# Kernel optimization log

Hardware: AMD Instinct MI355X
Metric: run time of the kernel (lower is better)

Reference implementation:

```python
import jax, jax.numpy as jnp
import numpy as np

B, L, H, NL, O = 16, 96, 256, 2, 32  # batch, window len, hidden, layers, horizon


def setup_inputs() -> dict:
    key = jax.random.key(0)
    ks = jax.random.split(key, 12)
    s = 1.0 / np.sqrt(H)  # torch LSTM/Linear init scale
    u = lambda k, shp: jax.random.uniform(k, shp, jnp.float32, -s, s)
    return dict(
        x_enc=jax.random.normal(ks[0], (B, L, 1), jnp.float32),
        x_mark_enc=jnp.zeros((1,), jnp.float32),
        x_dec=jnp.zeros((1,), jnp.float32),
        x_mark_dec=jnp.zeros((1,), jnp.float32),
        Wih0=u(ks[1], (4 * H, 1)), Whh0=u(ks[2], (4 * H, H)),
        bih0=u(ks[3], (4 * H,)), bhh0=u(ks[4], (4 * H,)),
        Wih1=u(ks[5], (4 * H, H)), Whh1=u(ks[6], (4 * H, H)),
        bih1=u(ks[7], (4 * H,)), bhh1=u(ks[8], (4 * H,)),
        fc_w=u(ks[9], (1, H)), fc_b=u(ks[10], (1,)),
    )


def _lstm(x, h, c, params):
    """Multi-layer LSTM over x [B,T,in]; h,c: [NL,B,H]. Returns final (h,c).
    Only the final hidden state is needed (out[:, -1] == h[-1])."""
    def cell(carry, x_t):
        h, c = carry
        inp = x_t
        hs, cs = [], []
        for l, (Wih, Whh, bih, bhh) in enumerate(params):
            gates = inp @ Wih.T + h[l] @ Whh.T + bih + bhh  # [B,4H], torch gate order i,f,g,o
            i, f, g, o = jnp.split(gates, 4, axis=-1)
            cn = jax.nn.sigmoid(f) * c[l] + jax.nn.sigmoid(i) * jnp.tanh(g)
            hn = jax.nn.sigmoid(o) * jnp.tanh(cn)
            hs.append(hn); cs.append(cn)
            inp = hn
        return (jnp.stack(hs), jnp.stack(cs)), None
    (h, c), _ = jax.lax.scan(jax.checkpoint(cell), (h, c), jnp.swapaxes(x, 0, 1))
    return h, c


def reference(x_enc, x_mark_enc, x_dec, x_mark_dec,
              Wih0, Whh0, bih0, bhh0, Wih1, Whh1, bih1, bhh1, fc_w, fc_b):
    params = ((Wih0, Whh0, bih0, bhh0), (Wih1, Whh1, bih1, bhh1))
    b, l = x_enc.shape[0], x_enc.shape[1]
    h0 = jnp.zeros((NL, b, H), x_enc.dtype)
    # warm-up pass over the full encoder window (output discarded, state kept)
    h, c = _lstm(x_enc, h0, h0, params)

    def step(carry, _):
        h, c, win = carry
        h, c = _lstm(win, h, c, params)          # re-run LSTM over full rolling window
        pred = h[-1] @ fc_w.T + fc_b              # [B,1]
        win = jnp.concatenate([win[:, 1:], pred[:, None, :]], axis=1)
        return (h, c, win), pred

    _, preds = jax.lax.scan(step, (h, c, x_enc), None, length=O)  # [O,B,1]
    out = jnp.zeros((b, l, 1), x_enc.dtype).at[:, :O, :].set(jnp.swapaxes(preds, 0, 1))
    return out
```

## Files before the change

kernel.cpp:

```cpp
#include <hip/hip_runtime.h>


#define NWG 96
#define LASTP 3169

__device__ __forceinline__ float sigm(float x) { return 1.0f / (1.0f + expf(-x)); }

__global__ void init_kernel(float* __restrict__ out, float* __restrict__ ws) {
  int i = blockIdx.x * blockDim.x + threadIdx.x;
  if (i < 16 * 96) out[i] = 0.0f;
  for (int j = i; j < 17056; j += gridDim.x * blockDim.x) ws[j] = 0.0f;
}

__global__ __launch_bounds__(256, 1) void lstm_coop(
    const float* __restrict__ x_enc,
    const float* __restrict__ Wih0, const float* __restrict__ Whh0,
    const float* __restrict__ bih0, const float* __restrict__ bhh0,
    const float* __restrict__ Wih1, const float* __restrict__ Whh1,
    const float* __restrict__ bih1, const float* __restrict__ bhh1,
    const float* __restrict__ fc_w, const float* __restrict__ fc_b,
    float* __restrict__ out, float* __restrict__ ws) {
  const int w = blockIdx.x;
  const int tid = threadIdx.x;
  const int wave = tid >> 6, lane = tid & 63;
  const int b = lane & 15, q = lane >> 4;

  float* h0buf = ws;
  float* h1buf = ws + 8192;
  float* predbuf = ws + 16384;
  unsigned* bar = (unsigned*)(ws + 17024);

  __shared__ float wlds[32 * 272];

  const bool isL0 = (w < 32);
  const int u = w - 32;

  if (isL0) {
    for (int i = 0; i < 32; ++i) {
      int r_w = i & 7, wv = i >> 3;
      int col = w * 8 + wv * 2 + (r_w >> 2), gate = r_w & 3;
      wlds[i * 272 + (tid >> 6) * 68 + (tid & 63)] = Whh0[(gate * 256 + col) * 256 + tid];
    }
  } else {
    for (int i = 0; i < 32; ++i) {
      int r_w = i & 7, wv = i >> 3;
      int col = u * 4 + wv, gate = r_w & 3;
      const float* Wsrc = (r_w >> 2) ? Whh1 : Wih1;
      wlds[i * 272 + (tid >> 6) * 68 + (tid & 63)] = Wsrc[(gate * 256 + col) * 256 + tid];
    }
  }

  float biasv[8], xw[8];
  if (isL0) {
#pragma unroll
    for (int r = 0; r < 8; ++r) {
      int col = w * 8 + wave * 2 + (r >> 2), gate = r & 3;
      int grow = gate * 256 + col;
      biasv[r] = bih0[grow] + bhh0[grow];
      xw[r] = Wih0[grow];
    }
  } else {
#pragma unroll
    for (int g = 0; g < 4; ++g) {
      int col = u * 4 + wave;
      int grow = g * 256 + col;
      biasv[g] = bih1[grow] + bhh1[grow];
      xw[g] = 0.0f;
    }
#pragma unroll
    for (int g = 4; g < 8; ++g) { biasv[g] = 0.0f; xw[g] = 0.0f; }
  }
  __syncthreads();

  double c0a = 0.0, c0b = 0.0, c1 = 0.0;
  const int colBaseL0 = w * 8 + wave * 2;
  const int colL1 = u * 4 + wave;

  for (int p = 0; p <= LASTP; ++p) {
    if (isL0) {
      if (p <= 3167) {
        const float* hsrc = h0buf + ((p + 1) & 1) * 4096 + b * 256 + q * 64;
        float h[64];
#pragma unroll
        for (int jj = 0; jj < 16; ++jj) {
          float4 v = *(const float4*)(hsrc + jj * 4);
          h[jj * 4 + 0] = v.x; h[jj * 4 + 1] = v.y; h[jj * 4 + 2] = v.z; h[jj * 4 + 3] = v.w;
        }
        float acc[8];
#pragma unroll
        for (int r = 0; r < 8; ++r) acc[r] = 0.0f;
#pragma unroll
        for (int r = 0; r < 8; ++r) {
          int base = (wave * 8 + r) * 272 + q * 68;
#pragma unroll
          for (int jj = 0; jj < 16; ++jj) {
            float4 wv = *(const float4*)&wlds[base + jj * 4];
            acc[r] += wv.x * h[jj * 4] + wv.y * h[jj * 4 + 1] + wv.z * h[jj * 4 + 2] + wv.w * h[jj * 4 + 3];
          }
        }
#pragma unroll
        for (int r = 0; r < 8; ++r) {
          acc[r] += __shfl_xor(acc[r], 16);
          acc[r] += __shfl_xor(acc[r], 32);
        }
        if (q == 0) {
          float xv;
          {
            int s = p;
            if (s < 96) {
              xv = x_enc[b * 96 + s];
            } else {
              int sk = s - 96;
              int k = sk / 96;
              int t = sk - k * 96;
              xv = (t < 96 - k) ? x_enc[b * 96 + k + t] : predbuf[(t - 96 + k) * 16 + b];
            }
          }
          float hv0, hv1;
          {
            float gi = acc[0] + xv * xw[0] + biasv[0];
            float gf = acc[1] + xv * xw[1] + biasv[1];
            float gg = acc[2] + xv * xw[2] + biasv[2];
            float go = acc[3] + xv * xw[3] + biasv[3];
            double cn = (double)sigm(gf) * c0a + (double)(sigm(gi) * tanhf(gg));
            hv0 = sigm(go) * tanhf((float)cn);
            c0a = cn;
          }
          {
            float gi = acc[4] + xv * xw[4] + biasv[4];
            float gf = acc[5] + xv * xw[5] + biasv[5];
            float gg = acc[6] + xv * xw[6] + biasv[6];
            float go = acc[7] + xv * xw[7] + biasv[7];
            double cn = (double)sigm(gf) * c0b + (double)(sigm(gi) * tanhf(gg));
            hv1 = sigm(go) * tanhf((float)cn);
            c0b = cn;
          }
          *(float2*)(h0buf + (p & 1) * 4096 + b * 256 + colBaseL0) = make_float2(hv0, hv1);
        }
      }
      if (w == 0 && wave == 0 && p >= 193 && ((p - 193) % 96) == 0) {
        int jp = (p - 193) / 96;
        if (jp < 32) {
          const float* hsrc = h1buf + 4096 + b * 256 + q * 64;
          const float* fw = fc_w + q * 64;
          float acc = 0.0f;
#pragma unroll
          for (int jj = 0; jj < 16; ++jj) {
            float4 hv = *(const float4*)(hsrc + jj * 4);
            float4 wv = *(const float4*)(fw + jj * 4);
            acc += hv.x * wv.x + hv.y * wv.y + hv.z * wv.z + hv.w * wv.w;
          }
          acc += __shfl_xor(acc, 16);
          acc += __shfl_xor(acc, 32);
          if (q == 0) {
            float pv = acc + fc_b[0];
            predbuf[jp * 16 + b] = pv;
            out[b * 96 + jp] = pv;
          }
        }
      }
    } else {
      if (p >= 1 && p <= 3168) {
        const float* h0src = h0buf + ((p + 1) & 1) * 4096 + b * 256 + q * 64;
        const float* h1src = h1buf + (p & 1) * 4096 + b * 256 + q * 64;
        float ha[64], hb[64];
#pragma unroll
        for (int jj = 0; jj < 16; ++jj) {
          float4 v = *(const float4*)(h0src + jj * 4);
          ha[jj * 4 + 0] = v.x; ha[jj * 4 + 1] = v.y; ha[jj * 4 + 2] = v.z; ha[jj * 4 + 3] = v.w;
        }
#pragma unroll
        for (int jj = 0; jj < 16; ++jj) {
          float4 v = *(const float4*)(h1src + jj * 4);
          hb[jj * 4 + 0] = v.x; hb[jj * 4 + 1] = v.y; hb[jj * 4 + 2] = v.z; hb[jj * 4 + 3] = v.w;
        }
        float acc[8];
#pragma unroll
        for (int r = 0; r < 8; ++r) acc[r] = 0.0f;
#pragma unroll
        for (int r = 0; r < 4; ++r) {
          int base = (wave * 8 + r) * 272 + q * 68;
#pragma unroll
          for (int jj = 0; jj < 16; ++jj) {
            float4 wv = *(const float4*)&wlds[base + jj * 4];
            acc[r] += wv.x * ha[jj * 4] + wv.y * ha[jj * 4 + 1] + wv.z * ha[jj * 4 + 2] + wv.w * ha[jj * 4 + 3];
          }
        }
#pragma unroll
        for (int r = 4; r < 8; ++r) {
          int base = (wave * 8 + r) * 272 + q * 68;
#pragma unroll
          for (int jj = 0; jj < 16; ++jj) {
            float4 wv = *(const float4*)&wlds[base + jj * 4];
            acc[r] += wv.x * hb[jj * 4] + wv.y * hb[jj * 4 + 1] + wv.z * hb[jj * 4 + 2] + wv.w * hb[jj * 4 + 3];
          }
        }
#pragma unroll
        for (int r = 0; r < 8; ++r) {
          acc[r] += __shfl_xor(acc[r], 16);
          acc[r] += __shfl_xor(acc[r], 32);
        }
        if (q == 0) {
          float gi = acc[0] + acc[4] + biasv[0];
          float gf = acc[1] + acc[5] + biasv[1];
          float gg = acc[2] + acc[6] + biasv[2];
          float go = acc[3] + acc[7] + biasv[3];
          double cn = (double)sigm(gf) * c1 + (double)(sigm(gi) * tanhf(gg));
          float hn = sigm(go) * tanhf((float)cn);
          c1 = cn;
          h1buf[((p + 1) & 1) * 4096 + b * 256 + colL1] = hn;
        }
      }
    }

    __syncthreads();
    if (tid == 0) {
      unsigned arrived = __hip_atomic_fetch_add(&bar[0], 1u, __ATOMIC_ACQ_REL, __HIP_MEMORY_SCOPE_AGENT);
      if (arrived == NWG - 1) {
        __hip_atomic_store(&bar[0], 0u, __ATOMIC_RELAXED, __HIP_MEMORY_SCOPE_AGENT);
        __hip_atomic_store(&bar[1], (unsigned)(p + 1), __ATOMIC_RELEASE, __HIP_MEMORY_SCOPE_AGENT);
      } else {
        while (__hip_atomic_load(&bar[1], __ATOMIC_RELAXED, __HIP_MEMORY_SCOPE_AGENT) < (unsigned)(p + 1)) {}
        __threadfence();
      }
    }
    __syncthreads();
  }
}

extern "C" void kernel_launch(void* const* d_in, const int* in_sizes, int n_in,
                              void* d_out, int out_size, void* d_ws, size_t ws_size,
                              hipStream_t stream) {
  const float* x_enc = (const float*)d_in[0];
  const float* Wih0 = (const float*)d_in[4];
  const float* Whh0 = (const float*)d_in[5];
  const float* bih0 = (const float*)d_in[6];
  const float* bhh0 = (const float*)d_in[7];
  const float* Wih1 = (const float*)d_in[8];
  const float* Whh1 = (const float*)d_in[9];
  const float* bih1 = (const float*)d_in[10];
  const float* bhh1 = (const float*)d_in[11];
  const float* fc_w = (const float*)d_in[12];
  const float* fc_b = (const float*)d_in[13];
  float* out = (float*)d_out;
  float* ws = (float*)d_ws;

  hipLaunchKernelGGL(init_kernel, dim3(8), dim3(256), 0, stream, out, ws);

  void* args[] = {&x_enc, &Wih0, &Whh0, &bih0, &bhh0, &Wih1, &Whh1, &bih1, &bhh1,
                  &fc_w, &fc_b, &out, &ws};
  (void)hipLaunchCooperativeKernel((void*)lstm_coop, dim3(NWG), dim3(256), args, 0u, stream);
}
```

Baseline: 39.13 ms.

## Consolidate LSTM into 24 larger workgroups with flag-based grid barrier

Cuts the persistent cooperative grid from 96 workgroups of 256 threads to 24 workgroups of 1024 threads, each holding four times as many weight rows in dynamic LDS. The central atomic-counter barrier becomes per-workgroup padded flags that one wave polls with a wave-wide vote. The inner matvec loops are reordered to stream h in float4 chunks instead of staging 64-element register arrays. The aim is a cheaper per-step global barrier across thousands of sequential steps and lower register pressure, at the cost of fewer CUs sharing the work and more LDS per workgroup.

New measurement: 57.31 ms. 46.4% more time.

```diff
diff --git a/kernel.cpp b/kernel.cpp
--- a/kernel.cpp
+++ b/kernel.cpp
@@ -1,7 +1,7 @@
 #include <hip/hip_runtime.h>
 
 
-#define NWG 96
+#define NWG 24
 #define LASTP 3169
 
 __device__ __forceinline__ float sigm(float x) { return 1.0f / (1.0f + expf(-x)); }
@@ -9,10 +9,10 @@
 __global__ void init_kernel(float* __restrict__ out, float* __restrict__ ws) {
   int i = blockIdx.x * blockDim.x + threadIdx.x;
   if (i < 16 * 96) out[i] = 0.0f;
-  for (int j = i; j < 17056; j += gridDim.x * blockDim.x) ws[j] = 0.0f;
+  for (int j = i; j < 17408; j += gridDim.x * blockDim.x) ws[j] = 0.0f;
 }
 
-__global__ __launch_bounds__(256, 1) void lstm_coop(
+extern "C" __global__ __launch_bounds__(1024, 1) void lstm_coop(
     const float* __restrict__ x_enc,
     const float* __restrict__ Wih0, const float* __restrict__ Whh0,
     const float* __restrict__ bih0, const float* __restrict__ bhh0,
@@ -28,25 +28,25 @@
   float* h0buf = ws;
   float* h1buf = ws + 8192;
   float* predbuf = ws + 16384;
-  unsigned* bar = (unsigned*)(ws + 17024);
-
-  __shared__ float wlds[32 * 272];
-
-  const bool isL0 = (w < 32);
-  const int u = w - 32;
-
-  if (isL0) {
-    for (int i = 0; i < 32; ++i) {
-      int r_w = i & 7, wv = i >> 3;
-      int col = w * 8 + wv * 2 + (r_w >> 2), gate = r_w & 3;
-      wlds[i * 272 + (tid >> 6) * 68 + (tid & 63)] = Whh0[(gate * 256 + col) * 256 + tid];
-    }
-  } else {
-    for (int i = 0; i < 32; ++i) {
-      int r_w = i & 7, wv = i >> 3;
-      int col = u * 4 + wv, gate = r_w & 3;
-      const float* Wsrc = (r_w >> 2) ? Whh1 : Wih1;
-      wlds[i * 272 + (tid >> 6) * 68 + (tid & 63)] = Wsrc[(gate * 256 + col) * 256 + tid];
+  unsigned* flags = (unsigned*)(ws + 17024);
+
+  extern __shared__ float wlds[];
+
+  const bool isL0 = (w < 8);
+  const int u = w - 8;
+
+  for (int e = tid; e < 128 * 256; e += 1024) {
+    int row = e >> 8;
+    int k = e & 255;
+    int wv = row >> 3, r = row & 7;
+    int dst = row * 272 + (k >> 6) * 68 + (k & 63);
+    if (isL0) {
+      int col = w * 32 + wv * 2 + (r >> 2), gate = r & 3;
+      wlds[dst] = Whh0[(gate * 256 + col) * 256 + k];
+    } else {
+      int col = u * 16 + wv, gate = r & 3;
+      const float* Wsrc = (r >= 4) ? Whh1 : Wih1;
+      wlds[dst] = Wsrc[(gate * 256 + col) * 256 + k];
     }
   }
 
@@ -54,7 +54,7 @@
   if (isL0) {
 #pragma unroll
     for (int r = 0; r < 8; ++r) {
-      int col = w * 8 + wave * 2 + (r >> 2), gate = r & 3;
+      int col = w * 32 + wave * 2 + (r >> 2), gate = r & 3;
       int grow = gate * 256 + col;
       biasv[r] = bih0[grow] + bhh0[grow];
       xw[r] = Wih0[grow];
@@ -62,7 +62,7 @@
   } else {
 #pragma unroll
     for (int g = 0; g < 4; ++g) {
-      int col = u * 4 + wave;
+      int col = u * 16 + wave;
       int grow = g * 256 + col;
       biasv[g] = bih1[grow] + bhh1[grow];
       xw[g] = 0.0f;
@@ -73,29 +73,24 @@
   __syncthreads();
 
   double c0a = 0.0, c0b = 0.0, c1 = 0.0;
-  const int colBaseL0 = w * 8 + wave * 2;
-  const int colL1 = u * 4 + wave;
+  const int colBaseL0 = w * 32 + wave * 2;
+  const int colL1 = u * 16 + wave;
 
   for (int p = 0; p <= LASTP; ++p) {
     if (isL0) {
       if (p <= 3167) {
         const float* hsrc = h0buf + ((p + 1) & 1) * 4096 + b * 256 + q * 64;
-        float h[64];
+        float acc[8];
+#pragma unroll
+        for (int r = 0; r < 8; ++r) acc[r] = 0.0f;
+        const int rbase = wave * 8 * 272 + q * 68;
 #pragma unroll
         for (int jj = 0; jj < 16; ++jj) {
-          float4 v = *(const float4*)(hsrc + jj * 4);
-          h[jj * 4 + 0] = v.x; h[jj * 4 + 1] = v.y; h[jj * 4 + 2] = v.z; h[jj * 4 + 3] = v.w;
-        }
-        float acc[8];
-#pragma unroll
-        for (int r = 0; r < 8; ++r) acc[r] = 0.0f;
-#pragma unroll
-        for (int r = 0; r < 8; ++r) {
-          int base = (wave * 8 + r) * 272 + q * 68;
-#pragma unroll
-          for (int jj = 0; jj < 16; ++jj) {
-            float4 wv = *(const float4*)&wlds[base + jj * 4];
-            acc[r] += wv.x * h[jj * 4] + wv.y * h[jj * 4 + 1] + wv.z * h[jj * 4 + 2] + wv.w * h[jj * 4 + 3];
+          float4 hv = *(const float4*)(hsrc + jj * 4);
+#pragma unroll
+          for (int r = 0; r < 8; ++r) {
+            float4 wv = *(const float4*)&wlds[rbase + r * 272 + jj * 4];
+            acc[r] += wv.x * hv.x + wv.y * hv.y + wv.z * hv.z + wv.w * hv.w;
           }
         }
 #pragma unroll
@@ -163,36 +158,23 @@
       if (p >= 1 && p <= 3168) {
         const float* h0src = h0buf + ((p + 1) & 1) * 4096 + b * 256 + q * 64;
         const float* h1src = h1buf + (p & 1) * 4096 + b * 256 + q * 64;
-        float ha[64], hb[64];
+        float acc[8];
+#pragma unroll
+        for (int r = 0; r < 8; ++r) acc[r] = 0.0f;
+        const int rbase = wave * 8 * 272 + q * 68;
 #pragma unroll
         for (int jj = 0; jj < 16; ++jj) {
-          float4 v = *(const float4*)(h0src + jj * 4);
-          ha[jj * 4 + 0] = v.x; ha[jj * 4 + 1] = v.y; ha[jj * 4 + 2] = v.z; ha[jj * 4 + 3] = v.w;
-        }
-#pragma unroll
-        for (int jj = 0; jj < 16; ++jj) {
-          float4 v = *(const float4*)(h1src + jj * 4);
-          hb[jj * 4 + 0] = v.x; hb[jj * 4 + 1] = v.y; hb[jj * 4 + 2] = v.z; hb[jj * 4 + 3] = v.w;
-        }
-        float acc[8];
-#pragma unroll
-        for (int r = 0; r < 8; ++r) acc[r] = 0.0f;
-#pragma unroll
-        for (int r = 0; r < 4; ++r) {
-          int base = (wave * 8 + r) * 272 + q * 68;
-#pragma unroll
-          for (int jj = 0; jj < 16; ++jj) {
-            float4 wv = *(const float4*)&wlds[base + jj * 4];
-            acc[r] += wv.x * ha[jj * 4] + wv.y * ha[jj * 4 + 1] + wv.z * ha[jj * 4 + 2] + wv.w * ha[jj * 4 + 3];
-          }
-        }
-#pragma unroll
-        for (int r = 4; r < 8; ++r) {
-          int base = (wave * 8 + r) * 272 + q * 68;
-#pragma unroll
-          for (int jj = 0; jj < 16; ++jj) {
-            float4 wv = *(const float4*)&wlds[base + jj * 4];
-            acc[r] += wv.x * hb[jj * 4] + wv.y * hb[jj * 4 + 1] + wv.z * hb[jj * 4 + 2] + wv.w * hb[jj * 4 + 3];
+          float4 h0v = *(const float4*)(h0src + jj * 4);
+          float4 h1v = *(const float4*)(h1src + jj * 4);
+#pragma unroll
+          for (int r = 0; r < 4; ++r) {
+            float4 wv = *(const float4*)&wlds[rbase + r * 272 + jj * 4];
+            acc[r] += wv.x * h0v.x + wv.y * h0v.y + wv.z * h0v.z + wv.w * h0v.w;
+          }
+#pragma unroll
+          for (int r = 4; r < 8; ++r) {
+            float4 wv = *(const float4*)&wlds[rbase + r * 272 + jj * 4];
+            acc[r] += wv.x * h1v.x + wv.y * h1v.y + wv.z * h1v.z + wv.w * h1v.w;
           }
         }
 #pragma unroll
@@ -215,14 +197,18 @@
 
     __syncthreads();
     if (tid == 0) {
-      unsigned arrived = __hip_atomic_fetch_add(&bar[0], 1u, __ATOMIC_ACQ_REL, __HIP_MEMORY_SCOPE_AGENT);
-      if (arrived == NWG - 1) {
-        __hip_atomic_store(&bar[0], 0u, __ATOMIC_RELAXED, __HIP_MEMORY_SCOPE_AGENT);
-        __hip_atomic_store(&bar[1], (unsigned)(p + 1), __ATOMIC_RELEASE, __HIP_MEMORY_SCOPE_AGENT);
-      } else {
-        while (__hip_atomic_load(&bar[1], __ATOMIC_RELAXED, __HIP_MEMORY_SCOPE_AGENT) < (unsigned)(p + 1)) {}
-        __threadfence();
-      }
+      __hip_atomic_store(&flags[w * 16], (unsigned)(p + 1), __ATOMIC_RELEASE,
+                         __HIP_MEMORY_SCOPE_AGENT);
+    }
+    if (wave == 0) {
+      const bool active = lane < NWG;
+      unsigned* myf = flags + (active ? lane : 0) * 16;
+      const unsigned tgt = (unsigned)(p + 1);
+      while (!__all(!active ||
+                    __hip_atomic_load(myf, __ATOMIC_RELAXED,
+                                      __HIP_MEMORY_SCOPE_AGENT) >= tgt)) {
+      }
+      __threadfence();
     }
     __syncthreads();
   }
@@ -247,7 +233,16 @@
 
   hipLaunchKernelGGL(init_kernel, dim3(8), dim3(256), 0, stream, out, ws);
 
+  const int ldsBytes = 128 * 272 * 4;
+  static int attrSet = 0;
+  if (!attrSet) {
+    (void)hipFuncSetAttribute((const void*)lstm_coop,
+                              hipFuncAttributeMaxDynamicSharedMemorySize, ldsBytes);
+    attrSet = 1;
+  }
+
   void* args[] = {&x_enc, &Wih0, &Whh0, &bih0, &bhh0, &Wih1, &Whh1, &bih1, &bhh1,
                   &fc_w, &fc_b, &out, &ws};
-  (void)hipLaunchCooperativeKernel((void*)lstm_coop, dim3(NWG), dim3(256), args, 0u, stream);
+  (void)hipLaunchCooperativeKernel((void*)lstm_coop, dim3(NWG), dim3(1024), args,
+                                   (unsigned)ldsBytes, stream);
 }
```
